# Kernel tuning notes

Measured on AMD Instinct MI355X. Metric: run time of the kernel, lower is better.

The kernel has to match this reference:

```python
import jax, jax.numpy as jnp
import numpy as np


def _edt(fg):
    """Exact 2D Euclidean distance transform.

    fg: [B, H, W] bool, True = foreground. Returns, for every pixel, the
    Euclidean distance to the nearest background (False) pixel; 0 on
    background pixels. Matches scipy.ndimage.distance_transform_edt.
    Two-pass separable algorithm: exact 1D city-block distance along axis 1,
    then exact lower-envelope min along axis 2 via a scan over columns.
    """
    B, H, W = fg.shape
    BIG = jnp.float32(H + W)  # larger than any achievable distance
    bg = ~fg
    row_idx = jnp.arange(H, dtype=jnp.float32)[None, :, None]  # [1,H,1]

    def dist_to_prev_bg(bg_mask):
        # distance (along axis 1) to the most recent background pixel above
        last = jax.lax.cummax(jnp.where(bg_mask, row_idx, -BIG), axis=1)
        return row_idx - last

    d_up = dist_to_prev_bg(bg)
    d_down = jnp.flip(dist_to_prev_bg(jnp.flip(bg, axis=1)), axis=1)
    g = jnp.minimum(jnp.minimum(d_up, d_down), BIG)  # [B,H,W] 1D vertical dist
    g2 = g * g

    # Second pass: D2[b,h,x] = min_{x'} g2[b,h,x'] + (x - x')^2  (exact EDT^2)
    x = jnp.arange(W, dtype=jnp.float32)  # [W]

    def body(D2, inp):
        xp, g2col = inp  # scalar, [B,H]
        cand = g2col[:, :, None] + (x - xp) ** 2  # [B,H,W]
        return jnp.minimum(D2, cand), None

    D2_init = jnp.full((B, H, W), (2.0 * BIG) ** 2, dtype=jnp.float32)
    D2, _ = jax.lax.scan(body, D2_init, (x, jnp.moveaxis(g2, 2, 0)))
    return jnp.sqrt(D2)


def setup_inputs() -> dict:
    key = jax.random.key(0)
    k1, k2 = jax.random.split(key)
    B, C, H, W = 8, 4, 256, 256
    logits = jax.random.normal(k1, (B, C, H, W), dtype=jnp.float32)
    pred_softmax = jax.nn.softmax(logits, axis=1)
    mask = jax.random.randint(k2, (B, H, W), 0, C, dtype=jnp.int64)
    return {"pred_softmax": pred_softmax, "mask": mask}


def reference(pred_softmax, mask):
    B, C, H, W = pred_softmax.shape
    norm = np.float32(np.sqrt(H * H + W * W) + 1e-6)
    loss = jnp.float32(0.0)
    for c in range(1, C):  # small fixed number of classes
        fg = mask == c
        dist = _edt(fg) / norm  # [B,H,W]; all-zeros when class absent, as in ref
        loss = loss + jnp.mean(pred_softmax[:, c] * dist)
    return loss / max(C - 1, 1)
```

## Files before the change

### kernel.cpp

```cpp
#include <hip/hip_runtime.h>
#include <math.h>

#define B_    8
#define C_    4
#define H_    256
#define W_    256
#define NCLS  3
#define NROWS (NCLS * B_ * H_)
#define BIGVAL (1 << 26)

__global__ __launch_bounds__(256) void vert_g_kernel(const int* __restrict__ mask,
                                                     unsigned short* __restrict__ gbuf) {
    const int lane = threadIdx.x & 63;
    const int hc   = threadIdx.x >> 6;
    const int blk  = blockIdx.x;
    const int wt   = blk & 3;
    const int b    = (blk >> 2) & 7;
    const int c_i  = blk >> 5;
    const int cls  = c_i + 1;
    const int w    = (wt << 6) + lane;

    __shared__ int last_sh[4][64];
    __shared__ int first_sh[4][64];

    const int* mptr = mask + (b << 16) + (hc << 14) + w;
    unsigned long long bg = 0ull;
    #pragma unroll 8
    for (int i = 0; i < 64; ++i) {
        int m = mptr[i << 8];
        bg |= (unsigned long long)(m != cls) << i;
    }
    last_sh[hc][lane]  = bg ? ((hc << 6) + 63 - __builtin_clzll(bg)) : -512;
    first_sh[hc][lane] = bg ? ((hc << 6) + __builtin_ctzll(bg)) : (1 << 20);
    __syncthreads();

    int carry_up = -512;
    #pragma unroll
    for (int k = 0; k < 4; ++k)
        if (k < hc) carry_up = max(carry_up, last_sh[k][lane]);
    int carry_dn = 1 << 20;
    #pragma unroll
    for (int k = 0; k < 4; ++k)
        if (k > hc) carry_dn = min(carry_dn, first_sh[k][lane]);

    unsigned short* gout = gbuf + (((c_i << 3) + b) << 16) + (hc << 14) + w;
    #pragma unroll 4
    for (int i = 0; i < 64; ++i) {
        int h = (hc << 6) + i;
        unsigned long long le = bg & (~0ull >> (63 - i));
        int last = le ? ((hc << 6) + 63 - __builtin_clzll(le)) : carry_up;
        int du = h - last;
        unsigned long long ge = bg >> i;
        int first = ge ? (h + __builtin_ctzll(ge)) : carry_dn;
        int dd = first - h;
        int g = min(min(du, dd), 512);
        gout[i << 8] = (unsigned short)g;
    }
}

__global__ __launch_bounds__(256) void horiz_kernel(const unsigned short* __restrict__ gbuf,
                                                    const float* __restrict__ pred,
                                                    double* __restrict__ acc) {
    const int lane = threadIdx.x & 63;
    const int wv   = threadIdx.x >> 6;
    const int row  = blockIdx.x * 4 + wv;
    const int c_i  = row >> 11;
    const int b    = (row >> 8) & 7;
    const int h    = row & 255;
    const int cls  = c_i + 1;

    __shared__ __align__(16) int ext[4][512];
    __shared__ double wsum[4];

    const int x0 = lane << 2;
    ushort4 gv = *(const ushort4*)(gbuf + row * 256 + x0);
    int g0 = gv.x, g1 = gv.y, g2v = gv.z, g3 = gv.w;
    int q0 = g0 * g0, q1 = g1 * g1, q2 = g2v * g2v, q3 = g3 * g3;
    *(int4*)&ext[wv][128 + x0] = make_int4(q0, q1, q2, q3);
    ext[wv][lane]       = BIGVAL;
    ext[wv][64 + lane]  = BIGVAL;
    ext[wv][384 + lane] = BIGVAL;
    ext[wv][448 + lane] = BIGVAL;
    __syncthreads();

    int gm = max(max(g0, g1), max(g2v, g3));
    #pragma unroll
    for (int off = 32; off > 0; off >>= 1) gm = max(gm, __shfl_xor(gm, off, 64));
    const int R = gm - 1;

    int D2[4] = { q0, q1, q2, q3 };
    const int* e = &ext[wv][128];

    if (R >= 120) {
        for (int xp = 0; xp < 256; ++xp) {
            int s = e[xp];
            #pragma unroll
            for (int j = 0; j < 4; ++j) {
                int d = (x0 + j) - xp;
                int cand = s + d * d;
                D2[j] = (cand < D2[j]) ? cand : D2[j];
            }
        }
    } else if (R >= 1) {
        for (int o = 1; o <= R; ++o) {
            int oo = o * o;
            #pragma unroll
            for (int j = 0; j < 4; ++j) {
                int xj = x0 + j;
                int c1 = e[xj + o];
                int c2 = e[xj - o];
                int cm = (c1 < c2) ? c1 : c2;
                int cand = cm + oo;
                D2[j] = (cand < D2[j]) ? cand : D2[j];
            }
        }
    }

    const float* prow = pred + ((((b << 2) + cls) << 8) + h) * 256;
    float4 pv = *(const float4*)(prow + x0);
    double sum = sqrt((double)D2[0]) * (double)pv.x
               + sqrt((double)D2[1]) * (double)pv.y
               + sqrt((double)D2[2]) * (double)pv.z
               + sqrt((double)D2[3]) * (double)pv.w;
    #pragma unroll
    for (int off = 32; off > 0; off >>= 1) sum += __shfl_xor(sum, off, 64);
    if (lane == 0) wsum[wv] = sum;
    __syncthreads();
    if (threadIdx.x == 0)
        acc[blockIdx.x] = wsum[0] + wsum[1] + wsum[2] + wsum[3];
}

__global__ __launch_bounds__(64) void final_kernel(const double* __restrict__ acc,
                                                   float* __restrict__ out) {
    int lane = threadIdx.x;
    double s = 0.0;
    for (int i = lane; i < NROWS / 4; i += 64) s += acc[i];
    #pragma unroll
    for (int off = 32; off > 0; off >>= 1) s += __shfl_xor(s, off, 64);
    if (lane == 0) {
        double nd = sqrt(131072.0) + 1e-6;
        double norm = (double)(float)nd;
        out[0] = (float)(s / norm / ((double)NCLS * (double)(B_ * H_ * W_)));
    }
}

extern "C" void kernel_launch(void* const* d_in, const int* in_sizes, int n_in,
                              void* d_out, int out_size, void* d_ws, size_t ws_size,
                              hipStream_t stream) {
    const float* pred = (const float*)d_in[0];
    const int*   mask = (const int*)d_in[1];
    float* out = (float*)d_out;

    char* ws = (char*)d_ws;
    double* acc = (double*)ws;
    unsigned short* gbuf = (unsigned short*)(ws + 16384);

    vert_g_kernel<<<NCLS * 8 * 4, 256, 0, stream>>>(mask, gbuf);
    horiz_kernel<<<NROWS / 4, 256, 0, stream>>>(gbuf, pred, acc);
    final_kernel<<<1, 64, 0, stream>>>(acc, out);
}
```

Before: 76.13 us.

## Fold final reduction into horiz kernel via atomics and process four rows per wave

The separate final reduction kernel is removed. Each horiz block now atomically adds its partial sum to a global double accumulator, and the last block, found with an atomic counter, writes the normalized output. The accumulator and counter are zeroed inside the vertical kernel. The horiz kernel now launches 384 blocks, each wave processing four rows serially, which cuts the launch count and block count but lowers parallelism (384 blocks on many CUs) and makes the double-precision sum order nondeterministic.

```diff
diff --git a/kernel.cpp b/kernel.cpp
--- a/kernel.cpp
+++ b/kernel.cpp
@@ -7,10 +7,15 @@
 #define W_    256
 #define NCLS  3
 #define NROWS (NCLS * B_ * H_)
+#define HBLOCKS 384
 #define BIGVAL (1 << 26)
 
 __global__ __launch_bounds__(256) void vert_g_kernel(const int* __restrict__ mask,
-                                                     unsigned short* __restrict__ gbuf) {
+                                                     unsigned short* __restrict__ gbuf,
+                                                     double* __restrict__ acc,
+                                                     unsigned int* __restrict__ counter) {
+    if (blockIdx.x == 0 && threadIdx.x == 0) { *acc = 0.0; *counter = 0u; }
+
     const int lane = threadIdx.x & 63;
     const int hc   = threadIdx.x >> 6;
     const int blk  = blockIdx.x;
@@ -60,87 +65,92 @@
 
 __global__ __launch_bounds__(256) void horiz_kernel(const unsigned short* __restrict__ gbuf,
                                                     const float* __restrict__ pred,
-                                                    double* __restrict__ acc) {
+                                                    double* __restrict__ acc,
+                                                    unsigned int* __restrict__ counter,
+                                                    float* __restrict__ out) {
     const int lane = threadIdx.x & 63;
     const int wv   = threadIdx.x >> 6;
-    const int row  = blockIdx.x * 4 + wv;
-    const int c_i  = row >> 11;
-    const int b    = (row >> 8) & 7;
-    const int h    = row & 255;
-    const int cls  = c_i + 1;
 
     __shared__ __align__(16) int ext[4][512];
     __shared__ double wsum[4];
 
     const int x0 = lane << 2;
-    ushort4 gv = *(const ushort4*)(gbuf + row * 256 + x0);
-    int g0 = gv.x, g1 = gv.y, g2v = gv.z, g3 = gv.w;
-    int q0 = g0 * g0, q1 = g1 * g1, q2 = g2v * g2v, q3 = g3 * g3;
-    *(int4*)&ext[wv][128 + x0] = make_int4(q0, q1, q2, q3);
-    ext[wv][lane]       = BIGVAL;
-    ext[wv][64 + lane]  = BIGVAL;
-    ext[wv][384 + lane] = BIGVAL;
-    ext[wv][448 + lane] = BIGVAL;
-    __syncthreads();
+    double sum = 0.0;
 
-    int gm = max(max(g0, g1), max(g2v, g3));
-    #pragma unroll
-    for (int off = 32; off > 0; off >>= 1) gm = max(gm, __shfl_xor(gm, off, 64));
-    const int R = gm - 1;
+    for (int r = 0; r < 4; ++r) {
+        const int row = (blockIdx.x << 4) + (wv << 2) + r;
+        const int c_i = row >> 11;
+        const int b   = (row >> 8) & 7;
+        const int h   = row & 255;
+        const int cls = c_i + 1;
 
-    int D2[4] = { q0, q1, q2, q3 };
-    const int* e = &ext[wv][128];
+        ushort4 gv = *(const ushort4*)(gbuf + row * 256 + x0);
+        int g0 = gv.x, g1 = gv.y, g2v = gv.z, g3 = gv.w;
+        int q0 = g0 * g0, q1 = g1 * g1, q2 = g2v * g2v, q3 = g3 * g3;
+        *(int4*)&ext[wv][128 + x0] = make_int4(q0, q1, q2, q3);
+        ext[wv][lane]       = BIGVAL;
+        ext[wv][64 + lane]  = BIGVAL;
+        ext[wv][384 + lane] = BIGVAL;
+        ext[wv][448 + lane] = BIGVAL;
+        __syncthreads();
 
-    if (R >= 120) {
-        for (int xp = 0; xp < 256; ++xp) {
-            int s = e[xp];
-            #pragma unroll
-            for (int j = 0; j < 4; ++j) {
-                int d = (x0 + j) - xp;
-                int cand = s + d * d;
-                D2[j] = (cand < D2[j]) ? cand : D2[j];
+        int gm = max(max(g0, g1), max(g2v, g3));
+        #pragma unroll
+        for (int off = 32; off > 0; off >>= 1) gm = max(gm, __shfl_xor(gm, off, 64));
+        const int R = gm - 1;
+
+        int D2[4] = { q0, q1, q2, q3 };
+        const int* e = &ext[wv][128];
+
+        if (R >= 120) {
+            for (int xp = 0; xp < 256; ++xp) {
+                int s = e[xp];
+                #pragma unroll
+                for (int j = 0; j < 4; ++j) {
+                    int d = (x0 + j) - xp;
+                    int cand = s + d * d;
+                    D2[j] = (cand < D2[j]) ? cand : D2[j];
+                }
+            }
+        } else if (R >= 1) {
+            for (int o = 1; o <= R; ++o) {
+                int oo = o * o;
+                #pragma unroll
+                for (int j = 0; j < 4; ++j) {
+                    int xj = x0 + j;
+                    int c1 = e[xj + o];
+                    int c2 = e[xj - o];
+                    int cm = (c1 < c2) ? c1 : c2;
+                    int cand = cm + oo;
+                    D2[j] = (cand < D2[j]) ? cand : D2[j];
+                }
             }
         }
-    } else if (R >= 1) {
-        for (int o = 1; o <= R; ++o) {
-            int oo = o * o;
-            #pragma unroll
-            for (int j = 0; j < 4; ++j) {
-                int xj = x0 + j;
-                int c1 = e[xj + o];
-                int c2 = e[xj - o];
-                int cm = (c1 < c2) ? c1 : c2;
-                int cand = cm + oo;
-                D2[j] = (cand < D2[j]) ? cand : D2[j];
-            }
-        }
+
+        const float* prow = pred + ((((b << 2) + cls) << 8) + h) * 256;
+        float4 pv = *(const float4*)(prow + x0);
+        sum += sqrt((double)D2[0]) * (double)pv.x
+             + sqrt((double)D2[1]) * (double)pv.y
+             + sqrt((double)D2[2]) * (double)pv.z
+             + sqrt((double)D2[3]) * (double)pv.w;
+        __syncthreads();
     }
 
-    const float* prow = pred + ((((b << 2) + cls) << 8) + h) * 256;
-    float4 pv = *(const float4*)(prow + x0);
-    double sum = sqrt((double)D2[0]) * (double)pv.x
-               + sqrt((double)D2[1]) * (double)pv.y
-               + sqrt((double)D2[2]) * (double)pv.z
-               + sqrt((double)D2[3]) * (double)pv.w;
     #pragma unroll
     for (int off = 32; off > 0; off >>= 1) sum += __shfl_xor(sum, off, 64);
     if (lane == 0) wsum[wv] = sum;
     __syncthreads();
-    if (threadIdx.x == 0)
-        acc[blockIdx.x] = wsum[0] + wsum[1] + wsum[2] + wsum[3];
-}
-
-__global__ __launch_bounds__(64) void final_kernel(const double* __restrict__ acc,
-                                                   float* __restrict__ out) {
-    int lane = threadIdx.x;
-    double s = 0.0;
-    for (int i = lane; i < NROWS / 4; i += 64) s += acc[i];
-    #pragma unroll
-    for (int off = 32; off > 0; off >>= 1) s += __shfl_xor(s, off, 64);
-    if (lane == 0) {
-        double nd = sqrt(131072.0) + 1e-6;
-        double norm = (double)(float)nd;
-        out[0] = (float)(s / norm / ((double)NCLS * (double)(B_ * H_ * W_)));
+    if (threadIdx.x == 0) {
+        double total = wsum[0] + wsum[1] + wsum[2] + wsum[3];
+        atomicAdd(acc, total);
+        __threadfence();
+        unsigned int old = atomicAdd(counter, 1u);
+        if (old == (unsigned int)(HBLOCKS - 1)) {
+            double s = atomicAdd(acc, 0.0);
+            double nd = sqrt(131072.0) + 1e-6;
+            double norm = (double)(float)nd;
+            out[0] = (float)(s / norm / ((double)NCLS * (double)(B_ * H_ * W_)));
+        }
     }
 }
 
@@ -153,9 +163,9 @@
 
     char* ws = (char*)d_ws;
     double* acc = (double*)ws;
+    unsigned int* counter = (unsigned int*)(ws + 64);
     unsigned short* gbuf = (unsigned short*)(ws + 16384);
 
-    vert_g_kernel<<<NCLS * 8 * 4, 256, 0, stream>>>(mask, gbuf);
-    horiz_kernel<<<NROWS / 4, 256, 0, stream>>>(gbuf, pred, acc);
-    final_kernel<<<1, 64, 0, stream>>>(acc, out);
+    vert_g_kernel<<<NCLS * 8 * 4, 256, 0, stream>>>(mask, gbuf, acc, counter);
+    horiz_kernel<<<HBLOCKS, 256, 0, stream>>>(gbuf, pred, acc, counter, out);
 }
```

After: 80.04 us. 1.05x slower.

## Fuse vertical and horizontal EDT passes into one kernel via LDS

Applied to the files above, without the earlier changes.

Merges the vertical distance pass and the horizontal lower-envelope pass into a single kernel. Each block recomputes full-column background bitmasks for its 32-row tile and writes squared distances straight into shared memory, so the global intermediate buffer and one launch go away. It also moves from double to float sqrt and uses far fewer, larger blocks (192 blocks, 8 rows per wave). The cost is redundant mask reads (each block reads the whole 256-row column), 64KB of LDS per block, and less parallelism, which may lengthen the serial per-wave work.

```diff
diff --git a/kernel.cpp b/kernel.cpp
--- a/kernel.cpp
+++ b/kernel.cpp
@@ -6,138 +6,138 @@
 #define H_    256
 #define W_    256
 #define NCLS  3
-#define NROWS (NCLS * B_ * H_)
+#define NBLK  192
 #define BIGVAL (1 << 26)
 
-__global__ __launch_bounds__(256) void vert_g_kernel(const int* __restrict__ mask,
-                                                     unsigned short* __restrict__ gbuf) {
-    const int lane = threadIdx.x & 63;
-    const int hc   = threadIdx.x >> 6;
-    const int blk  = blockIdx.x;
-    const int wt   = blk & 3;
-    const int b    = (blk >> 2) & 7;
-    const int c_i  = blk >> 5;
-    const int cls  = c_i + 1;
-    const int w    = (wt << 6) + lane;
+__global__ __launch_bounds__(256) void fused_kernel(const int* __restrict__ mask,
+                                                    const float* __restrict__ pred,
+                                                    double* __restrict__ acc) {
+    __shared__ int lds[32 * 512];
+    double* wsum = (double*)lds;
 
-    __shared__ int last_sh[4][64];
-    __shared__ int first_sh[4][64];
+    const int t   = threadIdx.x;
+    const int blk = blockIdx.x;
+    const int c_i = blk >> 6;
+    const int b   = (blk >> 3) & 7;
+    const int rt  = blk & 7;
+    const int cls = c_i + 1;
 
-    const int* mptr = mask + (b << 16) + (hc << 14) + w;
-    unsigned long long bg = 0ull;
-    #pragma unroll 8
-    for (int i = 0; i < 64; ++i) {
-        int m = mptr[i << 8];
-        bg |= (unsigned long long)(m != cls) << i;
+    const int* mcol = mask + (b << 16) + t;
+    unsigned long long bg[4];
+    #pragma unroll
+    for (int k = 0; k < 4; ++k) {
+        int mm[64];
+        #pragma unroll
+        for (int i = 0; i < 64; ++i) mm[i] = mcol[((k << 6) + i) << 8];
+        unsigned long long v = 0ull;
+        #pragma unroll
+        for (int i = 0; i < 64; ++i) v |= (unsigned long long)(mm[i] != cls) << i;
+        bg[k] = v;
     }
-    last_sh[hc][lane]  = bg ? ((hc << 6) + 63 - __builtin_clzll(bg)) : -512;
-    first_sh[hc][lane] = bg ? ((hc << 6) + __builtin_ctzll(bg)) : (1 << 20);
-    __syncthreads();
-
+    int clast[4], cfirst[4];
+    #pragma unroll
+    for (int k = 0; k < 4; ++k) {
+        clast[k]  = bg[k] ? ((k << 6) + 63 - __builtin_clzll(bg[k])) : -512;
+        cfirst[k] = bg[k] ? ((k << 6) + __builtin_ctzll(bg[k])) : (1 << 20);
+    }
+    const int ci = rt >> 1;
     int carry_up = -512;
     #pragma unroll
-    for (int k = 0; k < 4; ++k)
-        if (k < hc) carry_up = max(carry_up, last_sh[k][lane]);
+    for (int k = 0; k < 4; ++k) if (k < ci) carry_up = max(carry_up, clast[k]);
     int carry_dn = 1 << 20;
     #pragma unroll
-    for (int k = 0; k < 4; ++k)
-        if (k > hc) carry_dn = min(carry_dn, first_sh[k][lane]);
+    for (int k = 0; k < 4; ++k) if (k > ci) carry_dn = min(carry_dn, cfirst[k]);
 
-    unsigned short* gout = gbuf + (((c_i << 3) + b) << 16) + (hc << 14) + w;
+    const unsigned long long bgc = bg[ci];
+    const int i0 = (rt & 1) << 5;
     #pragma unroll 4
-    for (int i = 0; i < 64; ++i) {
-        int h = (hc << 6) + i;
-        unsigned long long le = bg & (~0ull >> (63 - i));
-        int last = le ? ((hc << 6) + 63 - __builtin_clzll(le)) : carry_up;
+    for (int r = 0; r < 32; ++r) {
+        int ib = i0 + r;
+        int h  = (ci << 6) + ib;
+        unsigned long long le = bgc & (~0ull >> (63 - ib));
+        int last  = le ? ((ci << 6) + 63 - __builtin_clzll(le)) : carry_up;
         int du = h - last;
-        unsigned long long ge = bg >> i;
+        unsigned long long ge = bgc >> ib;
         int first = ge ? (h + __builtin_ctzll(ge)) : carry_dn;
         int dd = first - h;
         int g = min(min(du, dd), 512);
-        gout[i << 8] = (unsigned short)g;
+        lds[r * 512 + 128 + t] = g * g;
     }
-}
-
-__global__ __launch_bounds__(256) void horiz_kernel(const unsigned short* __restrict__ gbuf,
-                                                    const float* __restrict__ pred,
-                                                    double* __restrict__ acc) {
-    const int lane = threadIdx.x & 63;
-    const int wv   = threadIdx.x >> 6;
-    const int row  = blockIdx.x * 4 + wv;
-    const int c_i  = row >> 11;
-    const int b    = (row >> 8) & 7;
-    const int h    = row & 255;
-    const int cls  = c_i + 1;
-
-    __shared__ __align__(16) int ext[4][512];
-    __shared__ double wsum[4];
-
-    const int x0 = lane << 2;
-    ushort4 gv = *(const ushort4*)(gbuf + row * 256 + x0);
-    int g0 = gv.x, g1 = gv.y, g2v = gv.z, g3 = gv.w;
-    int q0 = g0 * g0, q1 = g1 * g1, q2 = g2v * g2v, q3 = g3 * g3;
-    *(int4*)&ext[wv][128 + x0] = make_int4(q0, q1, q2, q3);
-    ext[wv][lane]       = BIGVAL;
-    ext[wv][64 + lane]  = BIGVAL;
-    ext[wv][384 + lane] = BIGVAL;
-    ext[wv][448 + lane] = BIGVAL;
+    const int pi = (t < 128) ? t : (256 + t);
+    #pragma unroll 4
+    for (int r = 0; r < 32; ++r) lds[r * 512 + pi] = BIGVAL;
     __syncthreads();
 
-    int gm = max(max(g0, g1), max(g2v, g3));
+    const int lane = t & 63;
+    const int wv   = t >> 6;
+    const int x0   = lane << 2;
+
+    const int pbase = (((b << 2) + cls) << 16) + (rt << 13) + (wv << 11) + x0;
+    float4 pv[8];
     #pragma unroll
-    for (int off = 32; off > 0; off >>= 1) gm = max(gm, __shfl_xor(gm, off, 64));
-    const int R = gm - 1;
+    for (int rr = 0; rr < 8; ++rr) pv[rr] = *(const float4*)(pred + pbase + (rr << 8));
 
-    int D2[4] = { q0, q1, q2, q3 };
-    const int* e = &ext[wv][128];
+    double sum = 0.0;
+    #pragma unroll 1
+    for (int rr = 0; rr < 8; ++rr) {
+        const int* e = &lds[((wv << 3) + rr) * 512 + 128];
+        int4 q = *(const int4*)&e[x0];
+        int D2[4] = { q.x, q.y, q.z, q.w };
 
-    if (R >= 120) {
-        for (int xp = 0; xp < 256; ++xp) {
-            int s = e[xp];
-            #pragma unroll
-            for (int j = 0; j < 4; ++j) {
-                int d = (x0 + j) - xp;
-                int cand = s + d * d;
-                D2[j] = (cand < D2[j]) ? cand : D2[j];
+        int mq = max(max(q.x, q.y), max(q.z, q.w));
+        #pragma unroll
+        for (int off = 32; off > 0; off >>= 1) mq = max(mq, __shfl_xor(mq, off, 64));
+        int gmax = (int)sqrtf((float)mq);
+        gmax = (gmax * gmax > mq) ? gmax - 1 : gmax;
+        gmax = ((gmax + 1) * (gmax + 1) <= mq) ? gmax + 1 : gmax;
+        const int R = gmax - 1;
+
+        if (R >= 120) {
+            for (int xp = 0; xp < 256; ++xp) {
+                int s = e[xp];
+                #pragma unroll
+                for (int j = 0; j < 4; ++j) {
+                    int d = (x0 + j) - xp;
+                    int cand = s + d * d;
+                    D2[j] = (cand < D2[j]) ? cand : D2[j];
+                }
+            }
+        } else if (R >= 1) {
+            for (int o = 1; o <= R; ++o) {
+                int oo = o * o;
+                #pragma unroll
+                for (int j = 0; j < 4; ++j) {
+                    int xj = x0 + j;
+                    int c1 = e[xj + o];
+                    int c2 = e[xj - o];
+                    int cm = (c1 < c2) ? c1 : c2;
+                    int cand = cm + oo;
+                    D2[j] = (cand < D2[j]) ? cand : D2[j];
+                }
             }
         }
-    } else if (R >= 1) {
-        for (int o = 1; o <= R; ++o) {
-            int oo = o * o;
-            #pragma unroll
-            for (int j = 0; j < 4; ++j) {
-                int xj = x0 + j;
-                int c1 = e[xj + o];
-                int c2 = e[xj - o];
-                int cm = (c1 < c2) ? c1 : c2;
-                int cand = cm + oo;
-                D2[j] = (cand < D2[j]) ? cand : D2[j];
-            }
-        }
+
+        sum += (double)(sqrtf((float)D2[0]) * pv[rr].x)
+             + (double)(sqrtf((float)D2[1]) * pv[rr].y)
+             + (double)(sqrtf((float)D2[2]) * pv[rr].z)
+             + (double)(sqrtf((float)D2[3]) * pv[rr].w);
     }
 
-    const float* prow = pred + ((((b << 2) + cls) << 8) + h) * 256;
-    float4 pv = *(const float4*)(prow + x0);
-    double sum = sqrt((double)D2[0]) * (double)pv.x
-               + sqrt((double)D2[1]) * (double)pv.y
-               + sqrt((double)D2[2]) * (double)pv.z
-               + sqrt((double)D2[3]) * (double)pv.w;
     #pragma unroll
     for (int off = 32; off > 0; off >>= 1) sum += __shfl_xor(sum, off, 64);
     if (lane == 0) wsum[wv] = sum;
     __syncthreads();
-    if (threadIdx.x == 0)
-        acc[blockIdx.x] = wsum[0] + wsum[1] + wsum[2] + wsum[3];
+    if (t == 0)
+        acc[blk] = wsum[0] + wsum[1] + wsum[2] + wsum[3];
 }
 
 __global__ __launch_bounds__(64) void final_kernel(const double* __restrict__ acc,
                                                    float* __restrict__ out) {
-    int lane = threadIdx.x;
-    double s = 0.0;
-    for (int i = lane; i < NROWS / 4; i += 64) s += acc[i];
+    const int t = threadIdx.x;
+    double s = acc[t] + acc[t + 64] + acc[t + 128];
     #pragma unroll
     for (int off = 32; off > 0; off >>= 1) s += __shfl_xor(s, off, 64);
-    if (lane == 0) {
+    if (t == 0) {
         double nd = sqrt(131072.0) + 1e-6;
         double norm = (double)(float)nd;
         out[0] = (float)(s / norm / ((double)NCLS * (double)(B_ * H_ * W_)));
@@ -151,11 +151,8 @@
     const int*   mask = (const int*)d_in[1];
     float* out = (float*)d_out;
 
-    char* ws = (char*)d_ws;
-    double* acc = (double*)ws;
-    unsigned short* gbuf = (unsigned short*)(ws + 16384);
+    double* acc = (double*)d_ws;
 
-    vert_g_kernel<<<NCLS * 8 * 4, 256, 0, stream>>>(mask, gbuf);
-    horiz_kernel<<<NROWS / 4, 256, 0, stream>>>(gbuf, pred, acc);
+    fused_kernel<<<NBLK, 256, 0, stream>>>(mask, pred, acc);
     final_kernel<<<1, 64, 0, stream>>>(acc, out);
 }
```

Result: no change. 76.03 us (-0.1%).
